# Optimization experiments

Measured on AMD Instinct MI355X. Metric: run time of the kernel, lower is better.

## Reference

```python
import jax, jax.numpy as jnp
import numpy as np

N_NODES = 50000
N_EDGES = 800000


def gcn_conv(x, edge_index, W, b):
    """PyG GCNConv: add self-loops, symmetric deg^{-1/2} normalization,
    dense transform, scatter-add aggregation."""
    n = x.shape[0]
    src, dst = edge_index[0], edge_index[1]
    # add self-loops
    loop = jnp.arange(n, dtype=src.dtype)
    src = jnp.concatenate([src, loop])
    dst = jnp.concatenate([dst, loop])
    # degree on destination nodes (includes self-loops -> deg >= 1)
    deg = jax.ops.segment_sum(jnp.ones_like(dst, dtype=x.dtype), dst, num_segments=n)
    dinv = jax.lax.rsqrt(deg)
    norm = dinv[src] * dinv[dst]  # [E+N]
    h = x @ W                     # [N, F_out] dense GEMM
    msg = h[src] * norm[:, None]  # gather + scale, [E+N, F_out]
    out = jax.ops.segment_sum(msg, dst, num_segments=n)  # scatter-add
    return out + b


def setup_inputs() -> dict:
    key = jax.random.key(0)
    ks = jax.random.split(key, 8)
    x = jax.random.normal(ks[0], (N_NODES, 100), dtype=jnp.float32)
    edge_index = jax.random.randint(ks[1], (2, N_EDGES), 0, N_NODES, dtype=jnp.int64)
    W1 = jax.random.normal(ks[2], (100, 256), dtype=jnp.float32) * 0.1
    b1 = jnp.zeros((256,), dtype=jnp.float32)
    W2 = jax.random.normal(ks[3], (256, 128), dtype=jnp.float32) * 0.06
    b2 = jnp.zeros((128,), dtype=jnp.float32)
    Wfc = jax.random.normal(ks[4], (128, 1), dtype=jnp.float32) * 0.09
    bfc = jnp.zeros((1,), dtype=jnp.float32)
    return {"x": x, "edge_index": edge_index, "W1": W1, "b1": b1,
            "W2": W2, "b2": b2, "Wfc": Wfc, "bfc": bfc}


def reference(x, edge_index, W1, b1, W2, b2, Wfc, bfc):
    # eval mode: F.dropout with training=False is identity
    h = jax.nn.relu(gcn_conv(x, edge_index, W1, b1))
    h = jax.nn.relu(gcn_conv(h, edge_index, W2, b2))
    return h @ Wfc + bfc  # [N, 1]
```

## Files before the change

### kernel.cpp

```cpp
#include <hip/hip_runtime.h>
#include <hip/hip_bf16.h>


#define F0 100
#define F1 256
#define F2 128
#define CAP 2048


__global__ void zero_i32(int* p, int n) {
    int i = blockIdx.x * blockDim.x + threadIdx.x;
    if (i < n) p[i] = 0;
}

__global__ void fill_f32(float* out, const float* __restrict__ bfc, int n) {
    int i = blockIdx.x * blockDim.x + threadIdx.x;
    if (i < n) out[i] = bfc[0];
}

__global__ void deg_count_i(const int* __restrict__ dst, int* deg, int e) {
    int i = blockIdx.x * blockDim.x + threadIdx.x;
    if (i < e) atomicAdd(deg + dst[i], 1);
}

__global__ __launch_bounds__(256) void scan1(const int* __restrict__ deg,
                                             int* __restrict__ excl,
                                             int* __restrict__ bsum,
                                             float* __restrict__ dinv, int n) {
    __shared__ int wsum[4];
    int i = blockIdx.x * 256 + threadIdx.x;
    int lane = threadIdx.x & 63, wid = threadIdx.x >> 6;
    int v = (i < n) ? deg[i] : 0;
    if (i < n) dinv[i] = rsqrtf((float)(v + 1));
    int s = v;
#pragma unroll
    for (int off = 1; off < 64; off <<= 1) {
        int t = __shfl_up(s, off, 64);
        if (lane >= off) s += t;
    }
    if (lane == 63) wsum[wid] = s;
    __syncthreads();
    int add = 0;
    for (int w = 0; w < wid; w++) add += wsum[w];
    if (i < n) excl[i] = add + s - v;
    if (threadIdx.x == 255) bsum[blockIdx.x] = add + s;
}

__global__ __launch_bounds__(256) void scan2(int* __restrict__ bsum, int nb,
                                             int* __restrict__ rowptr, int n) {
    __shared__ int wsum[4];
    int lane = threadIdx.x & 63, wid = threadIdx.x >> 6;
    int v = (threadIdx.x < nb) ? bsum[threadIdx.x] : 0;
    int s = v;
#pragma unroll
    for (int off = 1; off < 64; off <<= 1) {
        int t = __shfl_up(s, off, 64);
        if (lane >= off) s += t;
    }
    if (lane == 63) wsum[wid] = s;
    __syncthreads();
    int add = 0;
    for (int w = 0; w < wid; w++) add += wsum[w];
    if (threadIdx.x < nb) bsum[threadIdx.x] = add + s - v;
    if (threadIdx.x == 255) rowptr[n] = add + s;
}

__global__ void scan3(const int* __restrict__ excl, const int* __restrict__ bsum,
                      int* __restrict__ rowptr, int* __restrict__ cursor, int n) {
    int i = blockIdx.x * 256 + threadIdx.x;
    if (i < n) {
        int r = excl[i] + bsum[blockIdx.x];
        rowptr[i] = r;
        cursor[i] = r;
    }
}

__global__ void csr_fill(const int* __restrict__ src, const int* __restrict__ dst,
                         int* cursor, int* __restrict__ csr, int e) {
    int i = blockIdx.x * blockDim.x + threadIdx.x;
    if (i < e) {
        int pos = atomicAdd(cursor + dst[i], 1);
        csr[pos] = src[i];
    }
}

__global__ void scale_x(const float4* __restrict__ x4,
                        const float* __restrict__ dinv,
                        float4* __restrict__ xs4, int n25) {
    int i = blockIdx.x * blockDim.x + threadIdx.x;
    if (i < n25) {
        float d = dinv[i / 25];
        float4 v = x4[i];
        v.x *= d; v.y *= d; v.z *= d; v.w *= d;
        xs4[i] = v;
    }
}


__global__ __launch_bounds__(256) void pull_f100(
        const float* __restrict__ xs, const int* __restrict__ rowptr,
        const int* __restrict__ csr, const float* __restrict__ dinv,
        float* __restrict__ agg, int n) {
    int wave = threadIdx.x >> 6, lane = threadIdx.x & 63;
    int v = blockIdx.x * 4 + wave;
    if (v >= n) return;
    int beg = rowptr[v], end = rowptr[v + 1];
    float dv = dinv[v];
    int half = lane >> 5, q = lane & 31;
    bool act = q < 25;
    float4 acc = {0.f, 0.f, 0.f, 0.f};
    if (half == 0 && act) acc = ((const float4*)(xs + (size_t)v * F0))[q];

    for (int base = beg; base < end; base += 64) {
        int cnt = min(64, end - base);
        int sidx = (lane < cnt) ? csr[base + lane] : 0;
        int npf = cnt >> 1;
        int p = 0;
        for (; p + 4 <= npf; p += 4) {
            int s0 = __shfl(sidx, 2 * p + half, 64);
            int s1 = __shfl(sidx, 2 * p + 2 + half, 64);
            int s2 = __shfl(sidx, 2 * p + 4 + half, 64);
            int s3 = __shfl(sidx, 2 * p + 6 + half, 64);
            if (act) {
                float4 r0 = ((const float4*)(xs + (size_t)s0 * F0))[q];
                float4 r1 = ((const float4*)(xs + (size_t)s1 * F0))[q];
                float4 r2 = ((const float4*)(xs + (size_t)s2 * F0))[q];
                float4 r3 = ((const float4*)(xs + (size_t)s3 * F0))[q];
                acc.x += (r0.x + r1.x) + (r2.x + r3.x);
                acc.y += (r0.y + r1.y) + (r2.y + r3.y);
                acc.z += (r0.z + r1.z) + (r2.z + r3.z);
                acc.w += (r0.w + r1.w) + (r2.w + r3.w);
            }
        }
        for (; p < npf; p++) {
            int s0 = __shfl(sidx, 2 * p + half, 64);
            if (act) {
                float4 r0 = ((const float4*)(xs + (size_t)s0 * F0))[q];
                acc.x += r0.x; acc.y += r0.y; acc.z += r0.z; acc.w += r0.w;
            }
        }
        if (cnt & 1) {
            int sl = __shfl(sidx, cnt - 1, 64);
            if (half == 0 && act) {
                float4 r = ((const float4*)(xs + (size_t)sl * F0))[q];
                acc.x += r.x; acc.y += r.y; acc.z += r.z; acc.w += r.w;
            }
        }
    }
    float ox = __shfl_down(acc.x, 32, 64);
    float oy = __shfl_down(acc.y, 32, 64);
    float oz = __shfl_down(acc.z, 32, 64);
    float ow = __shfl_down(acc.w, 32, 64);
    if (half == 0 && act) {
        float4 r;
        r.x = dv * (acc.x + ox);
        r.y = dv * (acc.y + oy);
        r.z = dv * (acc.z + oz);
        r.w = dv * (acc.w + ow);
        ((float4*)(agg + (size_t)v * F0))[q] = r;
    }
}

__global__ __launch_bounds__(256) void pull_c16_fused(
        const float* __restrict__ h2c, const int* __restrict__ rowptr,
        const int* __restrict__ csr, const float* __restrict__ dinv,
        const float* __restrict__ b2, const float* __restrict__ Wfc,
        float* __restrict__ out, int n) {
    __shared__ int s_row[65];
    __shared__ float s_dinv[64];
    __shared__ int s_csr[CAP];
    int chunk = blockIdx.x & 7;
    int nb = blockIdx.x >> 3;
    int v0 = nb * 64;
    int tid = threadIdx.x;
    int lane = tid & 63, wv = tid >> 6;
    int q = lane & 3;
    int g2 = (lane >> 2) & 3;
    int grp = lane >> 4;
    const float* __restrict__ tab = h2c + (size_t)chunk * n * 16;

    if (tid <= 64) s_row[tid] = rowptr[min(v0 + tid, n)];
    if (tid < 64) s_dinv[tid] = (v0 + tid < n) ? dinv[v0 + tid] : 0.f;
    __syncthreads();
    int ebeg = s_row[0], eend = s_row[64];

    int base_local = wv * 16 + grp * 4;

    float4 acc[4];
#pragma unroll
    for (int nn = 0; nn < 4; ++nn) acc[nn] = (float4){0.f, 0.f, 0.f, 0.f};

#pragma unroll
    for (int nn = 0; nn < 4; ++nn) {
        int node = v0 + base_local + nn;
        if (node < n && g2 == 0)
            acc[nn] = ((const float4*)(tab + (size_t)node * 16))[q];
    }

    for (int w0 = ebeg; w0 < eend; w0 += CAP) {
        int wcnt = min(CAP, eend - w0);
        if (w0 != ebeg) __syncthreads();
        for (int i = tid; i < wcnt; i += 256)
            s_csr[i] = __builtin_nontemporal_load(csr + w0 + i);
        __syncthreads();
#pragma unroll
        for (int nn = 0; nn < 4; ++nn) {
            int local = base_local + nn;
            int nbg = max(s_row[local], w0) - w0;
            int nen = min(s_row[local + 1], w0 + wcnt) - w0;
            for (int t = nbg + 4 * g2; t < nen; t += 16) {
                int i1 = min(t + 1, nen - 1);
                int i2 = min(t + 2, nen - 1);
                int i3 = min(t + 3, nen - 1);
                int s0 = s_csr[t];
                int s1 = s_csr[i1];
                int s2 = s_csr[i2];
                int s3 = s_csr[i3];
                float4 r0 = ((const float4*)(tab + (size_t)s0 * 16))[q];
                float4 r1 = ((const float4*)(tab + (size_t)s1 * 16))[q];
                float4 r2 = ((const float4*)(tab + (size_t)s2 * 16))[q];
                float4 r3 = ((const float4*)(tab + (size_t)s3 * 16))[q];
                bool m1 = (t + 1 < nen), m2 = (t + 2 < nen), m3 = (t + 3 < nen);
                acc[nn].x += r0.x + (m1 ? r1.x : 0.f);
                acc[nn].y += r0.y + (m1 ? r1.y : 0.f);
                acc[nn].z += r0.z + (m1 ? r1.z : 0.f);
                acc[nn].w += r0.w + (m1 ? r1.w : 0.f);
                acc[nn].x += (m2 ? r2.x : 0.f) + (m3 ? r3.x : 0.f);
                acc[nn].y += (m2 ? r2.y : 0.f) + (m3 ? r3.y : 0.f);
                acc[nn].z += (m2 ? r2.z : 0.f) + (m3 ? r3.z : 0.f);
                acc[nn].w += (m2 ? r2.w : 0.f) + (m3 ? r3.w : 0.f);
            }
        }
    }

    int c0 = chunk * 16 + 4 * q;
    float4 bb = *(const float4*)(b2 + c0);
    float4 ww = *(const float4*)(Wfc + c0);
#pragma unroll
    for (int nn = 0; nn < 4; ++nn) {
        int local = base_local + nn;
        int node = v0 + local;
        float dv = s_dinv[local];
        float4 a = acc[nn];
        a.x += __shfl_xor(a.x, 4, 64);
        a.y += __shfl_xor(a.y, 4, 64);
        a.z += __shfl_xor(a.z, 4, 64);
        a.w += __shfl_xor(a.w, 4, 64);
        a.x += __shfl_xor(a.x, 8, 64);
        a.y += __shfl_xor(a.y, 8, 64);
        a.z += __shfl_xor(a.z, 8, 64);
        a.w += __shfl_xor(a.w, 8, 64);
        float part = fmaxf(fmaf(dv, a.x, bb.x), 0.f) * ww.x
                   + fmaxf(fmaf(dv, a.y, bb.y), 0.f) * ww.y
                   + fmaxf(fmaf(dv, a.z, bb.z), 0.f) * ww.z
                   + fmaxf(fmaf(dv, a.w, bb.w), 0.f) * ww.w;
        part += __shfl_xor(part, 1, 64);
        part += __shfl_xor(part, 2, 64);
        if (node < n && (lane & 15) == 0) atomicAdd(out + node, part);
    }
}


__global__ __launch_bounds__(256) void gemm1_tiled(
        const float* __restrict__ A, const float* __restrict__ W,
        const float* __restrict__ bias, float* __restrict__ C, int n) {
    __shared__ float As[20 * 128];
    __shared__ float Bs[20 * 128];
    int tid = threadIdx.x;
    int r0 = blockIdx.x * 128;
    int c0 = blockIdx.y * 128;
    int tc = tid & 15, tr = tid >> 4;
    float acc[8][8] = {};

    for (int k0 = 0; k0 < F0; k0 += 20) {
        if (k0) __syncthreads();
        for (int idx = tid; idx < 128 * 5; idx += 256) {
            int row = idx & 127, kq = idx >> 7;
            int gr = r0 + row;
            if (gr >= n) gr = n - 1;
            float4 v = *(const float4*)(A + (size_t)gr * F0 + k0 + 4 * kq);
            As[(4 * kq + 0) * 128 + row] = v.x;
            As[(4 * kq + 1) * 128 + row] = v.y;
            As[(4 * kq + 2) * 128 + row] = v.z;
            As[(4 * kq + 3) * 128 + row] = v.w;
        }
        for (int idx = tid; idx < 20 * 32; idx += 256) {
            int k = idx >> 5, cq = idx & 31;
            *(float4*)(Bs + k * 128 + 4 * cq) =
                *(const float4*)(W + (size_t)(k0 + k) * F1 + c0 + 4 * cq);
        }
        __syncthreads();
#pragma unroll 5
        for (int k = 0; k < 20; k++) {
            float4 a0 = *(const float4*)(As + k * 128 + 4 * tr);
            float4 a1 = *(const float4*)(As + k * 128 + 64 + 4 * tr);
            float4 b0 = *(const float4*)(Bs + k * 128 + 4 * tc);
            float4 b1 = *(const float4*)(Bs + k * 128 + 64 + 4 * tc);
            float av[8] = {a0.x, a0.y, a0.z, a0.w, a1.x, a1.y, a1.z, a1.w};
            float bv[8] = {b0.x, b0.y, b0.z, b0.w, b1.x, b1.y, b1.z, b1.w};
#pragma unroll
            for (int i = 0; i < 8; i++)
#pragma unroll
                for (int j = 0; j < 8; j++) acc[i][j] += av[i] * bv[j];
        }
    }
    float4 bb0 = *(const float4*)(bias + c0 + 4 * tc);
    float4 bb1 = *(const float4*)(bias + c0 + 64 + 4 * tc);
    float bv[8] = {bb0.x, bb0.y, bb0.z, bb0.w, bb1.x, bb1.y, bb1.z, bb1.w};
#pragma unroll
    for (int i = 0; i < 8; i++) {
        int row = (i < 4) ? (4 * tr + i) : (64 + 4 * tr + i - 4);
        int gr = r0 + row;
        if (gr < n) {
            float4 o0, o1;
            o0.x = fmaxf(acc[i][0] + bv[0], 0.f);
            o0.y = fmaxf(acc[i][1] + bv[1], 0.f);
            o0.z = fmaxf(acc[i][2] + bv[2], 0.f);
            o0.w = fmaxf(acc[i][3] + bv[3], 0.f);
            o1.x = fmaxf(acc[i][4] + bv[4], 0.f);
            o1.y = fmaxf(acc[i][5] + bv[5], 0.f);
            o1.z = fmaxf(acc[i][6] + bv[6], 0.f);
            o1.w = fmaxf(acc[i][7] + bv[7], 0.f);
            *(float4*)(C + (size_t)gr * F1 + c0 + 4 * tc) = o0;
            *(float4*)(C + (size_t)gr * F1 + c0 + 64 + 4 * tc) = o1;
        }
    }
}

__global__ __launch_bounds__(256) void gemm2_tiled(
        const float* __restrict__ A, const float* __restrict__ W,
        const float* __restrict__ dinv, float* __restrict__ C, int n) {
    __shared__ float As[32 * 128];
    __shared__ float Bs[32 * 128];
    int tid = threadIdx.x;
    int r0 = blockIdx.x * 128;
    int tc = tid & 15, tr = tid >> 4;
    float acc[8][8] = {};

    for (int k0 = 0; k0 < F1; k0 += 32) {
        if (k0) __syncthreads();
        for (int idx = tid; idx < 128 * 8; idx += 256) {
            int row = idx & 127, kq = idx >> 7;
            int gr = r0 + row;
            if (gr >= n) gr = n - 1;
            float4 v = *(const float4*)(A + (size_t)gr * F1 + k0 + 4 * kq);
            As[(4 * kq + 0) * 128 + row] = v.x;
            As[(4 * kq + 1) * 128 + row] = v.y;
            As[(4 * kq + 2) * 128 + row] = v.z;
            As[(4 * kq + 3) * 128 + row] = v.w;
        }
        for (int idx = tid; idx < 32 * 32; idx += 256) {
            int k = idx >> 5, cq = idx & 31;
            *(float4*)(Bs + k * 128 + 4 * cq) =
                *(const float4*)(W + (size_t)(k0 + k) * F2 + 4 * cq);
        }
        __syncthreads();
#pragma unroll 4
        for (int k = 0; k < 32; k++) {
            float4 a0 = *(const float4*)(As + k * 128 + 4 * tr);
            float4 a1 = *(const float4*)(As + k * 128 + 64 + 4 * tr);
            float4 b0 = *(const float4*)(Bs + k * 128 + 4 * tc);
            float4 b1 = *(const float4*)(Bs + k * 128 + 64 + 4 * tc);
            float av[8] = {a0.x, a0.y, a0.z, a0.w, a1.x, a1.y, a1.z, a1.w};
            float bv[8] = {b0.x, b0.y, b0.z, b0.w, b1.x, b1.y, b1.z, b1.w};
#pragma unroll
            for (int i = 0; i < 8; i++)
#pragma unroll
                for (int j = 0; j < 8; j++) acc[i][j] += av[i] * bv[j];
        }
    }
    int ch = tc >> 2;
    int of = (tc & 3) << 2;
#pragma unroll
    for (int i = 0; i < 8; i++) {
        int row = (i < 4) ? (4 * tr + i) : (64 + 4 * tr + i - 4);
        int gr = r0 + row;
        if (gr < n) {
            float d = dinv[gr];
            float4 o0 = {acc[i][0] * d, acc[i][1] * d, acc[i][2] * d, acc[i][3] * d};
            float4 o1 = {acc[i][4] * d, acc[i][5] * d, acc[i][6] * d, acc[i][7] * d};
            *(float4*)(C + ((size_t)ch * n + gr) * 16 + of) = o0;
            *(float4*)(C + ((size_t)(ch + 4) * n + gr) * 16 + of) = o1;
        }
    }
}


static inline size_t align16(size_t x) { return (x + 3) & ~(size_t)3; }

extern "C" void kernel_launch(void* const* d_in, const int* in_sizes, int n_in,
                              void* d_out, int out_size, void* d_ws, size_t ws_size,
                              hipStream_t stream) {
    const float* x   = (const float*)d_in[0];
    const int*   ei  = (const int*)d_in[1];
    const float* W1  = (const float*)d_in[2];
    const float* b1  = (const float*)d_in[3];
    const float* W2  = (const float*)d_in[4];
    const float* b2  = (const float*)d_in[5];
    const float* Wfc = (const float*)d_in[6];
    const float* bfc = (const float*)d_in[7];
    float* out = (float*)d_out;

    const int n = in_sizes[0] / F0;
    const int e = in_sizes[1] / 2;
    const int* src = ei;
    const int* dst = ei + e;

    char* wsb = (char*)d_ws;
    size_t off = 0;
    int* deg    = (int*)(wsb + 4 * off); off = align16(off + n);
    int* excl   = (int*)(wsb + 4 * off); off = align16(off + n);
    int* bsum   = (int*)(wsb + 4 * off); off = align16(off + 256);
    int* rowptr = (int*)(wsb + 4 * off); off = align16(off + n + 1);
    int* cursor = (int*)(wsb + 4 * off); off = align16(off + n);
    int* csr    = (int*)(wsb + 4 * off); off = align16(off + e);
    float* dinv = (float*)(wsb + 4 * off); off = align16(off + n);
    float* xs   = (float*)(wsb + 4 * off); off = align16(off + (size_t)n * F0);
    float* aggX = (float*)(wsb + 4 * off); off = align16(off + (size_t)n * F0);
    float* a1   = (float*)(wsb + 4 * off); off = align16(off + (size_t)n * F1);
    float* h2c  = (float*)(wsb + 4 * off); off = align16(off + (size_t)n * F2);

    const int B = 256;
    const int nb = (n + B - 1) / B;
    const int rblocks = (n + 127) / 128;

    zero_i32<<<nb, B, 0, stream>>>(deg, n);
    fill_f32<<<nb, B, 0, stream>>>(out, bfc, n);
    deg_count_i<<<(e + B - 1) / B, B, 0, stream>>>(dst, deg, e);
    scan1<<<nb, B, 0, stream>>>(deg, excl, bsum, dinv, n);
    scale_x<<<((n * 25) + B - 1) / B, B, 0, stream>>>(
        (const float4*)x, dinv, (float4*)xs, n * 25);
    scan2<<<1, B, 0, stream>>>(bsum, nb, rowptr, n);
    scan3<<<nb, B, 0, stream>>>(excl, bsum, rowptr, cursor, n);
    csr_fill<<<(e + B - 1) / B, B, 0, stream>>>(src, dst, cursor, csr, e);

    pull_f100<<<(n + 3) / 4, 256, 0, stream>>>(xs, rowptr, csr, dinv, aggX, n);
    gemm1_tiled<<<dim3(rblocks, F1 / 128), 256, 0, stream>>>(aggX, W1, b1, a1, n);

    gemm2_tiled<<<rblocks, 256, 0, stream>>>(a1, W2, dinv, h2c, n);
    pull_c16_fused<<<8 * ((n + 63) / 64), 256, 0, stream>>>(
        h2c, rowptr, csr, dinv, b2, Wfc, out, n);
}
```

Before: 389.5 us.

## Replace FP32 tiled GEMMs with split-FP16 MFMA GEMMs

Both dense transforms now run on matrix cores via mfma_f32_16x16x32_f16. Each FP32 operand is split into a high and a low fp16 part, and three MFMAs per tile approximate FP32 accuracy. The aggregation kernel and the first GEMM write their outputs in this hi/lo fp16 form, padded to 128 columns, and a new kernel pre-splits the weights. Workspace buffers are aliased to reuse memory. The aim is to replace scalar FMA-bound GEMM time with matrix-core throughput, at the cost of extra split/convert work and a small accuracy loss from the three-term split.

```diff
diff --git a/kernel.cpp b/kernel.cpp
--- a/kernel.cpp
+++ b/kernel.cpp
@@ -6,6 +6,10 @@
 #define F1 256
 #define F2 128
 #define CAP 2048
+
+typedef _Float16 f16x4 __attribute__((ext_vector_type(4)));
+typedef _Float16 f16x8 __attribute__((ext_vector_type(8)));
+typedef float f32x4 __attribute__((ext_vector_type(4)));
 
 
 __global__ void zero_i32(int* p, int n) {
@@ -96,11 +100,31 @@
     }
 }
 
+__global__ void wprep(const float* __restrict__ W1, const float* __restrict__ W2,
+                      _Float16* __restrict__ W1h, _Float16* __restrict__ W1l,
+                      _Float16* __restrict__ W2h, _Float16* __restrict__ W2l) {
+    int i = blockIdx.x * 256 + threadIdx.x;
+    if (i < 256 * 128) {
+        int c = i >> 7, k = i & 127;
+        float v = (k < F0) ? W1[(size_t)k * F1 + c] : 0.f;
+        _Float16 h = (_Float16)v;
+        W1h[i] = h;
+        W1l[i] = (_Float16)(v - (float)h);
+    } else if (i < 256 * 128 + 128 * 256) {
+        int j = i - 256 * 128;
+        int c = j >> 8, k = j & 255;
+        float v = W2[(size_t)k * F2 + c];
+        _Float16 h = (_Float16)v;
+        W2h[j] = h;
+        W2l[j] = (_Float16)(v - (float)h);
+    }
+}
+
 
 __global__ __launch_bounds__(256) void pull_f100(
         const float* __restrict__ xs, const int* __restrict__ rowptr,
         const int* __restrict__ csr, const float* __restrict__ dinv,
-        float* __restrict__ agg, int n) {
+        _Float16* __restrict__ aggh, _Float16* __restrict__ aggl, int n) {
     int wave = threadIdx.x >> 6, lane = threadIdx.x & 63;
     int v = blockIdx.x * 4 + wave;
     if (v >= n) return;
@@ -151,15 +175,147 @@
     float oy = __shfl_down(acc.y, 32, 64);
     float oz = __shfl_down(acc.z, 32, 64);
     float ow = __shfl_down(acc.w, 32, 64);
-    if (half == 0 && act) {
-        float4 r;
-        r.x = dv * (acc.x + ox);
-        r.y = dv * (acc.y + oy);
-        r.z = dv * (acc.z + oz);
-        r.w = dv * (acc.w + ow);
-        ((float4*)(agg + (size_t)v * F0))[q] = r;
-    }
-}
+    if (half == 0) {
+        float4 r = {0.f, 0.f, 0.f, 0.f};
+        if (act) {
+            r.x = dv * (acc.x + ox);
+            r.y = dv * (acc.y + oy);
+            r.z = dv * (acc.z + oz);
+            r.w = dv * (acc.w + ow);
+        }
+        f16x4 hh, ll;
+        hh[0] = (_Float16)r.x; ll[0] = (_Float16)(r.x - (float)hh[0]);
+        hh[1] = (_Float16)r.y; ll[1] = (_Float16)(r.y - (float)hh[1]);
+        hh[2] = (_Float16)r.z; ll[2] = (_Float16)(r.z - (float)hh[2]);
+        hh[3] = (_Float16)r.w; ll[3] = (_Float16)(r.w - (float)hh[3]);
+        *(f16x4*)(aggh + (size_t)v * 128 + 4 * q) = hh;
+        *(f16x4*)(aggl + (size_t)v * 128 + 4 * q) = ll;
+    }
+}
+
+
+__global__ __launch_bounds__(256) void gemm1_mfma(
+        const _Float16* __restrict__ Ah, const _Float16* __restrict__ Al,
+        const _Float16* __restrict__ Bh, const _Float16* __restrict__ Bl,
+        const float* __restrict__ bias,
+        _Float16* __restrict__ Ch, _Float16* __restrict__ Cl, int n) {
+    __shared__ _Float16 sAh[128][40], sAl[128][40], sBh[128][40], sBl[128][40];
+    int tid = threadIdx.x, lane = tid & 63, wave = tid >> 6;
+    int wm = wave >> 1, wn = wave & 1;
+    int r0 = blockIdx.x * 128, c0 = blockIdx.y * 128;
+    int lr = lane & 15, ks8 = (lane >> 4) * 8;
+    f32x4 acc[4][4] = {};
+
+    for (int k0 = 0; k0 < 128; k0 += 32) {
+        if (k0) __syncthreads();
+#pragma unroll
+        for (int p = 0; p < 2; ++p) {
+            int u = tid + p * 256;
+            int row = u >> 2, vv = u & 3;
+            int gr = min(r0 + row, n - 1);
+            *(f16x8*)&sAh[row][vv * 8] = *(const f16x8*)(Ah + (size_t)gr * 128 + k0 + vv * 8);
+            *(f16x8*)&sAl[row][vv * 8] = *(const f16x8*)(Al + (size_t)gr * 128 + k0 + vv * 8);
+            *(f16x8*)&sBh[row][vv * 8] = *(const f16x8*)(Bh + (size_t)(c0 + row) * 128 + k0 + vv * 8);
+            *(f16x8*)&sBl[row][vv * 8] = *(const f16x8*)(Bl + (size_t)(c0 + row) * 128 + k0 + vv * 8);
+        }
+        __syncthreads();
+        f16x8 a_h[4], a_l[4], b_h[4], b_l[4];
+#pragma unroll
+        for (int f = 0; f < 4; ++f) {
+            a_h[f] = *(const f16x8*)&sAh[wm * 64 + f * 16 + lr][ks8];
+            a_l[f] = *(const f16x8*)&sAl[wm * 64 + f * 16 + lr][ks8];
+            b_h[f] = *(const f16x8*)&sBh[wn * 64 + f * 16 + lr][ks8];
+            b_l[f] = *(const f16x8*)&sBl[wn * 64 + f * 16 + lr][ks8];
+        }
+#pragma unroll
+        for (int i = 0; i < 4; ++i)
+#pragma unroll
+            for (int j = 0; j < 4; ++j) {
+                acc[i][j] = __builtin_amdgcn_mfma_f32_16x16x32_f16(a_l[i], b_h[j], acc[i][j], 0, 0, 0);
+                acc[i][j] = __builtin_amdgcn_mfma_f32_16x16x32_f16(a_h[i], b_l[j], acc[i][j], 0, 0, 0);
+                acc[i][j] = __builtin_amdgcn_mfma_f32_16x16x32_f16(a_h[i], b_h[j], acc[i][j], 0, 0, 0);
+            }
+    }
+#pragma unroll
+    for (int j = 0; j < 4; ++j) {
+        int col = c0 + wn * 64 + j * 16 + lr;
+        float bv = bias[col];
+#pragma unroll
+        for (int i = 0; i < 4; ++i) {
+            int rbase = r0 + wm * 64 + i * 16 + (lane >> 4) * 4;
+#pragma unroll
+            for (int r = 0; r < 4; ++r) {
+                int gr = rbase + r;
+                if (gr < n) {
+                    float vv = fmaxf(acc[i][j][r] + bv, 0.f);
+                    _Float16 h = (_Float16)vv;
+                    Ch[(size_t)gr * 256 + col] = h;
+                    Cl[(size_t)gr * 256 + col] = (_Float16)(vv - (float)h);
+                }
+            }
+        }
+    }
+}
+
+__global__ __launch_bounds__(256) void gemm2_mfma(
+        const _Float16* __restrict__ Ah, const _Float16* __restrict__ Al,
+        const _Float16* __restrict__ Bh, const _Float16* __restrict__ Bl,
+        const float* __restrict__ dinv, float* __restrict__ C, int n) {
+    __shared__ _Float16 sAh[128][40], sAl[128][40], sBh[128][40], sBl[128][40];
+    int tid = threadIdx.x, lane = tid & 63, wave = tid >> 6;
+    int wm = wave >> 1, wn = wave & 1;
+    int r0 = blockIdx.x * 128;
+    int lr = lane & 15, ks8 = (lane >> 4) * 8;
+    f32x4 acc[4][4] = {};
+
+    for (int k0 = 0; k0 < 256; k0 += 32) {
+        if (k0) __syncthreads();
+#pragma unroll
+        for (int p = 0; p < 2; ++p) {
+            int u = tid + p * 256;
+            int row = u >> 2, vv = u & 3;
+            int gr = min(r0 + row, n - 1);
+            *(f16x8*)&sAh[row][vv * 8] = *(const f16x8*)(Ah + (size_t)gr * 256 + k0 + vv * 8);
+            *(f16x8*)&sAl[row][vv * 8] = *(const f16x8*)(Al + (size_t)gr * 256 + k0 + vv * 8);
+            *(f16x8*)&sBh[row][vv * 8] = *(const f16x8*)(Bh + (size_t)row * 256 + k0 + vv * 8);
+            *(f16x8*)&sBl[row][vv * 8] = *(const f16x8*)(Bl + (size_t)row * 256 + k0 + vv * 8);
+        }
+        __syncthreads();
+        f16x8 a_h[4], a_l[4], b_h[4], b_l[4];
+#pragma unroll
+        for (int f = 0; f < 4; ++f) {
+            a_h[f] = *(const f16x8*)&sAh[wm * 64 + f * 16 + lr][ks8];
+            a_l[f] = *(const f16x8*)&sAl[wm * 64 + f * 16 + lr][ks8];
+            b_h[f] = *(const f16x8*)&sBh[wn * 64 + f * 16 + lr][ks8];
+            b_l[f] = *(const f16x8*)&sBl[wn * 64 + f * 16 + lr][ks8];
+        }
+#pragma unroll
+        for (int i = 0; i < 4; ++i)
+#pragma unroll
+            for (int j = 0; j < 4; ++j) {
+                acc[i][j] = __builtin_amdgcn_mfma_f32_16x16x32_f16(a_l[i], b_h[j], acc[i][j], 0, 0, 0);
+                acc[i][j] = __builtin_amdgcn_mfma_f32_16x16x32_f16(a_h[i], b_l[j], acc[i][j], 0, 0, 0);
+                acc[i][j] = __builtin_amdgcn_mfma_f32_16x16x32_f16(a_h[i], b_h[j], acc[i][j], 0, 0, 0);
+            }
+    }
+#pragma unroll
+    for (int j = 0; j < 4; ++j) {
+        int chunk = wn * 4 + j;
+#pragma unroll
+        for (int i = 0; i < 4; ++i) {
+            int rbase = r0 + wm * 64 + i * 16 + (lane >> 4) * 4;
+#pragma unroll
+            for (int r = 0; r < 4; ++r) {
+                int gr = rbase + r;
+                if (gr < n) {
+                    float d = dinv[gr];
+                    C[((size_t)chunk * n + gr) * 16 + lr] = acc[i][j][r] * d;
+                }
+            }
+        }
+    }
+}
+
 
 __global__ __launch_bounds__(256) void pull_c16_fused(
         const float* __restrict__ h2c, const int* __restrict__ rowptr,
@@ -261,133 +417,6 @@
 }
 
 
-__global__ __launch_bounds__(256) void gemm1_tiled(
-        const float* __restrict__ A, const float* __restrict__ W,
-        const float* __restrict__ bias, float* __restrict__ C, int n) {
-    __shared__ float As[20 * 128];
-    __shared__ float Bs[20 * 128];
-    int tid = threadIdx.x;
-    int r0 = blockIdx.x * 128;
-    int c0 = blockIdx.y * 128;
-    int tc = tid & 15, tr = tid >> 4;
-    float acc[8][8] = {};
-
-    for (int k0 = 0; k0 < F0; k0 += 20) {
-        if (k0) __syncthreads();
-        for (int idx = tid; idx < 128 * 5; idx += 256) {
-            int row = idx & 127, kq = idx >> 7;
-            int gr = r0 + row;
-            if (gr >= n) gr = n - 1;
-            float4 v = *(const float4*)(A + (size_t)gr * F0 + k0 + 4 * kq);
-            As[(4 * kq + 0) * 128 + row] = v.x;
-            As[(4 * kq + 1) * 128 + row] = v.y;
-            As[(4 * kq + 2) * 128 + row] = v.z;
-            As[(4 * kq + 3) * 128 + row] = v.w;
-        }
-        for (int idx = tid; idx < 20 * 32; idx += 256) {
-            int k = idx >> 5, cq = idx & 31;
-            *(float4*)(Bs + k * 128 + 4 * cq) =
-                *(const float4*)(W + (size_t)(k0 + k) * F1 + c0 + 4 * cq);
-        }
-        __syncthreads();
-#pragma unroll 5
-        for (int k = 0; k < 20; k++) {
-            float4 a0 = *(const float4*)(As + k * 128 + 4 * tr);
-            float4 a1 = *(const float4*)(As + k * 128 + 64 + 4 * tr);
-            float4 b0 = *(const float4*)(Bs + k * 128 + 4 * tc);
-            float4 b1 = *(const float4*)(Bs + k * 128 + 64 + 4 * tc);
-            float av[8] = {a0.x, a0.y, a0.z, a0.w, a1.x, a1.y, a1.z, a1.w};
-            float bv[8] = {b0.x, b0.y, b0.z, b0.w, b1.x, b1.y, b1.z, b1.w};
-#pragma unroll
-            for (int i = 0; i < 8; i++)
-#pragma unroll
-                for (int j = 0; j < 8; j++) acc[i][j] += av[i] * bv[j];
-        }
-    }
-    float4 bb0 = *(const float4*)(bias + c0 + 4 * tc);
-    float4 bb1 = *(const float4*)(bias + c0 + 64 + 4 * tc);
-    float bv[8] = {bb0.x, bb0.y, bb0.z, bb0.w, bb1.x, bb1.y, bb1.z, bb1.w};
-#pragma unroll
-    for (int i = 0; i < 8; i++) {
-        int row = (i < 4) ? (4 * tr + i) : (64 + 4 * tr + i - 4);
-        int gr = r0 + row;
-        if (gr < n) {
-            float4 o0, o1;
-            o0.x = fmaxf(acc[i][0] + bv[0], 0.f);
-            o0.y = fmaxf(acc[i][1] + bv[1], 0.f);
-            o0.z = fmaxf(acc[i][2] + bv[2], 0.f);
-            o0.w = fmaxf(acc[i][3] + bv[3], 0.f);
-            o1.x = fmaxf(acc[i][4] + bv[4], 0.f);
-            o1.y = fmaxf(acc[i][5] + bv[5], 0.f);
-            o1.z = fmaxf(acc[i][6] + bv[6], 0.f);
-            o1.w = fmaxf(acc[i][7] + bv[7], 0.f);
-            *(float4*)(C + (size_t)gr * F1 + c0 + 4 * tc) = o0;
-            *(float4*)(C + (size_t)gr * F1 + c0 + 64 + 4 * tc) = o1;
-        }
-    }
-}
-
-__global__ __launch_bounds__(256) void gemm2_tiled(
-        const float* __restrict__ A, const float* __restrict__ W,
-        const float* __restrict__ dinv, float* __restrict__ C, int n) {
-    __shared__ float As[32 * 128];
-    __shared__ float Bs[32 * 128];
-    int tid = threadIdx.x;
-    int r0 = blockIdx.x * 128;
-    int tc = tid & 15, tr = tid >> 4;
-    float acc[8][8] = {};
-
-    for (int k0 = 0; k0 < F1; k0 += 32) {
-        if (k0) __syncthreads();
-        for (int idx = tid; idx < 128 * 8; idx += 256) {
-            int row = idx & 127, kq = idx >> 7;
-            int gr = r0 + row;
-            if (gr >= n) gr = n - 1;
-            float4 v = *(const float4*)(A + (size_t)gr * F1 + k0 + 4 * kq);
-            As[(4 * kq + 0) * 128 + row] = v.x;
-            As[(4 * kq + 1) * 128 + row] = v.y;
-            As[(4 * kq + 2) * 128 + row] = v.z;
-            As[(4 * kq + 3) * 128 + row] = v.w;
-        }
-        for (int idx = tid; idx < 32 * 32; idx += 256) {
-            int k = idx >> 5, cq = idx & 31;
-            *(float4*)(Bs + k * 128 + 4 * cq) =
-                *(const float4*)(W + (size_t)(k0 + k) * F2 + 4 * cq);
-        }
-        __syncthreads();
-#pragma unroll 4
-        for (int k = 0; k < 32; k++) {
-            float4 a0 = *(const float4*)(As + k * 128 + 4 * tr);
-            float4 a1 = *(const float4*)(As + k * 128 + 64 + 4 * tr);
-            float4 b0 = *(const float4*)(Bs + k * 128 + 4 * tc);
-            float4 b1 = *(const float4*)(Bs + k * 128 + 64 + 4 * tc);
-            float av[8] = {a0.x, a0.y, a0.z, a0.w, a1.x, a1.y, a1.z, a1.w};
-            float bv[8] = {b0.x, b0.y, b0.z, b0.w, b1.x, b1.y, b1.z, b1.w};
-#pragma unroll
-            for (int i = 0; i < 8; i++)
-#pragma unroll
-                for (int j = 0; j < 8; j++) acc[i][j] += av[i] * bv[j];
-        }
-    }
-    int ch = tc >> 2;
-    int of = (tc & 3) << 2;
-#pragma unroll
-    for (int i = 0; i < 8; i++) {
-        int row = (i < 4) ? (4 * tr + i) : (64 + 4 * tr + i - 4);
-        int gr = r0 + row;
-        if (gr < n) {
-            float d = dinv[gr];
-            float4 o0 = {acc[i][0] * d, acc[i][1] * d, acc[i][2] * d, acc[i][3] * d};
-            float4 o1 = {acc[i][4] * d, acc[i][5] * d, acc[i][6] * d, acc[i][7] * d};
-            *(float4*)(C + ((size_t)ch * n + gr) * 16 + of) = o0;
-            *(float4*)(C + ((size_t)(ch + 4) * n + gr) * 16 + of) = o1;
-        }
-    }
-}
-
-
-static inline size_t align16(size_t x) { return (x + 3) & ~(size_t)3; }
-
 extern "C" void kernel_launch(void* const* d_in, const int* in_sizes, int n_in,
                               void* d_out, int out_size, void* d_ws, size_t ws_size,
                               hipStream_t stream) {
@@ -408,17 +437,31 @@
 
     char* wsb = (char*)d_ws;
     size_t off = 0;
-    int* deg    = (int*)(wsb + 4 * off); off = align16(off + n);
-    int* excl   = (int*)(wsb + 4 * off); off = align16(off + n);
-    int* bsum   = (int*)(wsb + 4 * off); off = align16(off + 256);
-    int* rowptr = (int*)(wsb + 4 * off); off = align16(off + n + 1);
-    int* cursor = (int*)(wsb + 4 * off); off = align16(off + n);
-    int* csr    = (int*)(wsb + 4 * off); off = align16(off + e);
-    float* dinv = (float*)(wsb + 4 * off); off = align16(off + n);
-    float* xs   = (float*)(wsb + 4 * off); off = align16(off + (size_t)n * F0);
-    float* aggX = (float*)(wsb + 4 * off); off = align16(off + (size_t)n * F0);
-    float* a1   = (float*)(wsb + 4 * off); off = align16(off + (size_t)n * F1);
-    float* h2c  = (float*)(wsb + 4 * off); off = align16(off + (size_t)n * F2);
+    auto alloc = [&](size_t bytes) -> void* {
+        off = (off + 255) & ~(size_t)255;
+        void* r = wsb + off;
+        off += bytes;
+        return r;
+    };
+    int* deg    = (int*)alloc((size_t)n * 4);
+    int* excl   = (int*)alloc((size_t)n * 4);
+    int* bsum   = (int*)alloc(1024);
+    int* rowptr = (int*)alloc((size_t)(n + 1) * 4);
+    int* cursor = (int*)alloc((size_t)n * 4);
+    int* csr    = (int*)alloc((size_t)e * 4);
+    float* dinv = (float*)alloc((size_t)n * 4);
+    _Float16* W1h = (_Float16*)alloc(256 * 128 * 2);
+    _Float16* W1l = (_Float16*)alloc(256 * 128 * 2);
+    _Float16* W2h = (_Float16*)alloc(128 * 256 * 2);
+    _Float16* W2l = (_Float16*)alloc(128 * 256 * 2);
+    char* bufA = (char*)alloc((size_t)n * 256 * 2 * 2);
+    float* xs = (float*)bufA;
+    _Float16* a1h = (_Float16*)bufA;
+    _Float16* a1l = a1h + (size_t)n * 256;
+    char* bufB = (char*)alloc((size_t)n * 128 * 4);
+    _Float16* aggh = (_Float16*)bufB;
+    _Float16* aggl = aggh + (size_t)n * 128;
+    float* h2c = (float*)bufB;
 
     const int B = 256;
     const int nb = (n + B - 1) / B;
@@ -430,14 +473,15 @@
     scan1<<<nb, B, 0, stream>>>(deg, excl, bsum, dinv, n);
     scale_x<<<((n * 25) + B - 1) / B, B, 0, stream>>>(
         (const float4*)x, dinv, (float4*)xs, n * 25);
+    wprep<<<256, 256, 0, stream>>>(W1, W2, W1h, W1l, W2h, W2l);
     scan2<<<1, B, 0, stream>>>(bsum, nb, rowptr, n);
     scan3<<<nb, B, 0, stream>>>(excl, bsum, rowptr, cursor, n);
     csr_fill<<<(e + B - 1) / B, B, 0, stream>>>(src, dst, cursor, csr, e);
 
-    pull_f100<<<(n + 3) / 4, 256, 0, stream>>>(xs, rowptr, csr, dinv, aggX, n);
-    gemm1_tiled<<<dim3(rblocks, F1 / 128), 256, 0, stream>>>(aggX, W1, b1, a1, n);
-
-    gemm2_tiled<<<rblocks, 256, 0, stream>>>(a1, W2, dinv, h2c, n);
+    pull_f100<<<(n + 3) / 4, 256, 0, stream>>>(xs, rowptr, csr, dinv, aggh, aggl, n);
+    gemm1_mfma<<<dim3(rblocks, 2), 256, 0, stream>>>(aggh, aggl, W1h, W1l, b1,
+                                                     a1h, a1l, n);
+    gemm2_mfma<<<rblocks, 256, 0, stream>>>(a1h, a1l, W2h, W2l, dinv, h2c, n);
     pull_c16_fused<<<8 * ((n + 63) / 64), 256, 0, stream>>>(
         h2c, rowptr, csr, dinv, b2, Wfc, out, n);
 }
```

Measured after the change: 346.6 us. 1.12x faster.
